# Performance work log

Hardware: AMD Instinct MI355X
Metric: run time of the kernel (lower is better)

## Reference

```python
import jax, jax.numpy as jnp
import numpy as np

NUM_CLASSES = 81
THRESH_HI = 0.5
THRESH_LO = 0.4
GAMMA = 2.0
ALPHA = 0.25
VARIANCE = (0.1, 0.2)  # cfg['variance'] in ssd.pytorch
B, P, T = 32, 24564, 20


def setup_inputs() -> dict:
    key = jax.random.key(0)
    k1, k2, k3, k4, k5, k6, k7 = jax.random.split(key, 7)
    loc_data = jax.random.normal(k1, (B, P, 4), jnp.float32)
    conf_data = jax.random.normal(k2, (B, P, NUM_CLASSES), jnp.float32)
    # priors in center form (cx, cy, w, h), all in [0,1]
    pcxy = jax.random.uniform(k3, (P, 2), minval=0.05, maxval=0.95)
    pwh = jax.random.uniform(k4, (P, 2), minval=0.04, maxval=0.5)
    priors = jnp.concatenate([pcxy, pwh], axis=-1).astype(jnp.float32)
    # ground-truth boxes in point form (xmin, ymin, xmax, ymax) + label
    tcxy = jax.random.uniform(k5, (B, T, 2), minval=0.1, maxval=0.9)
    twh = jax.random.uniform(k6, (B, T, 2), minval=0.05, maxval=0.4)
    boxes = jnp.clip(jnp.concatenate([tcxy - twh / 2, tcxy + twh / 2], -1), 0.0, 1.0)
    labels = jax.random.randint(k7, (B, T), 0, NUM_CLASSES - 1).astype(jnp.float32)
    targets = jnp.concatenate([boxes, labels[..., None]], axis=-1)  # [B,T,5]
    return {"loc_data": loc_data, "conf_data": conf_data, "priors": priors, "targets": targets}


def point_form(pr):
    # center form -> (xmin,ymin,xmax,ymax)
    return jnp.concatenate([pr[:, :2] - pr[:, 2:] / 2, pr[:, :2] + pr[:, 2:] / 2], -1)


def jaccard(box_a, box_b):
    # box_a [T,4], box_b [P,4], both point form -> IoU [T,P]
    lt = jnp.maximum(box_a[:, None, :2], box_b[None, :, :2])
    rb = jnp.minimum(box_a[:, None, 2:], box_b[None, :, 2:])
    wh = jnp.clip(rb - lt, 0.0)
    inter = wh[..., 0] * wh[..., 1]
    area_a = ((box_a[:, 2] - box_a[:, 0]) * (box_a[:, 3] - box_a[:, 1]))[:, None]
    area_b = ((box_b[:, 2] - box_b[:, 0]) * (box_b[:, 3] - box_b[:, 1]))[None, :]
    return inter / (area_a + area_b - inter)


def encode(matched, priors):
    # matched [P,4] point form, priors [P,4] center form
    g_cxcy = ((matched[:, :2] + matched[:, 2:]) / 2 - priors[:, :2]) / (VARIANCE[0] * priors[:, 2:])
    g_wh = jnp.log((matched[:, 2:] - matched[:, :2]) / priors[:, 2:]) / VARIANCE[1]
    return jnp.concatenate([g_cxcy, g_wh], -1)


def match_one(truths, labels, priors):
    # truths [T,4] point form, labels [T], priors [P,4] center form
    ov = jaccard(truths, point_form(priors))          # [T,P]
    best_prior_idx = jnp.argmax(ov, axis=1)           # [T] best prior per gt
    best_truth_overlap = jnp.max(ov, axis=0)          # [P]
    best_truth_idx = jnp.argmax(ov, axis=0)           # [P]
    # ensure every gt box keeps its best prior
    best_truth_overlap = best_truth_overlap.at[best_prior_idx].set(2.0)
    best_truth_idx = best_truth_idx.at[best_prior_idx].set(jnp.arange(truths.shape[0]))
    matched = truths[best_truth_idx]                  # [P,4]
    conf = labels[best_truth_idx].astype(jnp.int32) + 1
    conf = jnp.where(best_truth_overlap < THRESH_HI, -1, conf)  # ignore band
    conf = jnp.where(best_truth_overlap < THRESH_LO, 0, conf)   # background
    return encode(matched, priors), conf


def reference(loc_data, conf_data, priors, targets):
    truths = targets[..., :4]
    labels = targets[..., 4]
    loc_t, conf_t = jax.vmap(lambda t, l: match_one(t, l, priors))(truths, labels)
    pos = conf_t > 0                                  # [B,P]
    # smooth L1 over positive priors (sum reduction)
    diff = loc_data - loc_t
    ad = jnp.abs(diff)
    sl1 = jnp.where(ad < 1.0, 0.5 * diff * diff, ad - 0.5)
    loss_l = jnp.sum(sl1 * pos[..., None])
    # focal loss over ALL locations (ignore conf==-1)
    logits = conf_data.reshape(-1, NUM_CLASSES)
    tgt = conf_t.reshape(-1)
    valid = tgt >= 0
    tgt_safe = jnp.where(valid, tgt, 0)
    logpt = jnp.take_along_axis(jax.nn.log_softmax(logits, -1), tgt_safe[:, None], 1)[:, 0]
    pt = jnp.exp(logpt)
    alpha_t = jnp.where(tgt > 0, ALPHA, 1.0 - ALPHA)
    fl = -alpha_t * (1.0 - pt) ** GAMMA * logpt
    loss_c = jnp.sum(jnp.where(valid, fl, 0.0))
    n = jnp.sum(pos).astype(loc_data.dtype)
    return loss_l / n, loss_c / n
```

## Files before the change

kernel.cpp:

```cpp
#include <hip/hip_runtime.h>

#define NCLS 81
#define BB 32
#define PP 24564
#define TT 20
#define BP_SEGS 8
#define BP_SEG 3072
#define KL_BLOCKS 1792
#define KL_ROWS 32
#define KL_CHUNKS ((BB * PP) / KL_ROWS)
#define KL_F4 ((KL_ROWS * NCLS) / 4)

#define GLOAD_LDS16(g, l)                                                  \
    __builtin_amdgcn_global_load_lds(                                      \
        (const __attribute__((address_space(1))) void*)(g),                \
        (__attribute__((address_space(3))) void*)(l), 16, 0, 0)

__global__ __launch_bounds__(1024)
void k_bp(const float* __restrict__ priors,
          const float* __restrict__ targets,
          unsigned long long* __restrict__ bp_part,
          unsigned long long* __restrict__ bovbt)
{
    const int seg = blockIdx.x;
    const int b = blockIdx.y;

    __shared__ float trb[TT * 5];
    __shared__ unsigned long long wred[TT][16];
    if (threadIdx.x < TT * 5) trb[threadIdx.x] = targets[b * TT * 5 + threadIdx.x];
    __syncthreads();

    float X1[3], Y1[3], X2[3], Y2[3], pa[3];
    unsigned int pkey[3];
    bool ok[3];
    #pragma unroll
    for (int j = 0; j < 3; ++j) {
        int p = seg * BP_SEG + j * 1024 + threadIdx.x;
        ok[j] = p < PP;
        float4 pr = ok[j] ? ((const float4*)priors)[p] : make_float4(1.f, 1.f, 0.f, 0.f);
        float hw = __fmul_rn(pr.z, 0.5f), hh = __fmul_rn(pr.w, 0.5f);
        X1[j] = __fsub_rn(pr.x, hw); Y1[j] = __fsub_rn(pr.y, hh);
        X2[j] = __fadd_rn(pr.x, hw); Y2[j] = __fadd_rn(pr.y, hh);
        pa[j] = __fmul_rn(__fsub_rn(X2[j], X1[j]), __fsub_rn(Y2[j], Y1[j]));
        pkey[j] = 0xFFFFFFFFu - (unsigned)p;
    }

    const int wv = threadIdx.x >> 6;
    const int lane = threadIdx.x & 63;

    unsigned long long bkey[3] = {0ull, 0ull, 0ull};

    for (int t = 0; t < TT; ++t) {
        float tx1 = trb[t * 5 + 0], ty1 = trb[t * 5 + 1];
        float tx2 = trb[t * 5 + 2], ty2 = trb[t * 5 + 3];
        float ta = __fmul_rn(__fsub_rn(tx2, tx1), __fsub_rn(ty2, ty1));

        unsigned long long best = 0ull;
        #pragma unroll
        for (int j = 0; j < 3; ++j) {
            float lx = fmaxf(tx1, X1[j]), ly = fmaxf(ty1, Y1[j]);
            float rx = fminf(tx2, X2[j]), ry = fminf(ty2, Y2[j]);
            float w = fmaxf(__fsub_rn(rx, lx), 0.0f);
            float h = fmaxf(__fsub_rn(ry, ly), 0.0f);
            float inter = __fmul_rn(w, h);
            float denom = __fsub_rn(__fadd_rn(ta, pa[j]), inter);
            float ov = __fdiv_rn(inter, denom);
            unsigned long long ovhi = (unsigned long long)__float_as_uint(ov) << 32;
            unsigned long long key = ok[j] ? (ovhi | pkey[j]) : 0ull;
            if (key > best) best = key;
            unsigned long long rowk = ovhi | (unsigned long long)(31 - t);
            if (rowk > bkey[j]) bkey[j] = rowk;
        }
        #pragma unroll
        for (int s = 32; s; s >>= 1) {
            unsigned long long o = __shfl_xor(best, s, 64);
            if (o > best) best = o;
        }
        if (lane == 0) wred[t][wv] = best;
    }

    #pragma unroll
    for (int j = 0; j < 3; ++j) {
        int p = seg * BP_SEG + j * 1024 + threadIdx.x;
        if (p < PP) bovbt[b * PP + p] = bkey[j];
    }

    __syncthreads();
    if (threadIdx.x < TT) {
        unsigned long long m = wred[threadIdx.x][0];
        #pragma unroll
        for (int w = 1; w < 16; ++w) if (wred[threadIdx.x][w] > m) m = wred[threadIdx.x][w];
        bp_part[(b * TT + threadIdx.x) * BP_SEGS + seg] = m;
    }
}

__global__ __launch_bounds__(256, 4)
void k_stream(const float* __restrict__ conf,
              const float* __restrict__ loc,
              const float* __restrict__ priors,
              const float* __restrict__ targets,
              const unsigned long long* __restrict__ bp_part,
              const unsigned long long* __restrict__ bovbt,
              float* __restrict__ pl, float* __restrict__ pn, float* __restrict__ pc)
{
    __shared__ float buf[2][KL_ROWS * NCLS];
    __shared__ float trbS[2][2][TT * 5];
    __shared__ unsigned int bpbS[2][2][TT];

    const int tid = threadIdx.x;
    const int w = tid >> 6;
    const int lane = tid & 63;
    const int rl = tid >> 3;
    const int k = tid & 7;
    const float4* conf4 = (const float4*)conf;

    auto stage = [&](int c, int bi) {
        const float4* src = conf4 + (size_t)c * KL_F4;
        float4* dst = (float4*)buf[bi];
        #pragma unroll
        for (int j = 0; j < 2; ++j) {
            int idx = j * 256 + w * 64 + lane;
            GLOAD_LDS16(src + idx, dst + idx);
        }
        if (tid < KL_F4 - 512) {
            int idx = 512 + tid;
            GLOAD_LDS16(src + idx, dst + idx);
        }
    };

    auto load_meta = [&](int c, int bi) {
        int r0 = c * KL_ROWS;
        int b0 = r0 / PP;
        int b1 = (r0 + KL_ROWS - 1) / PP;
        if (tid < 200) {
            int which = tid / 100;
            int i = tid - which * 100;
            int bb = which ? b1 : b0;
            trbS[bi][which][i] = targets[bb * 100 + i];
        } else if (tid < 240) {
            int q2 = tid - 200;
            int which = q2 / 20;
            int t = q2 - which * 20;
            int bb = which ? b1 : b0;
            const unsigned long long* q = bp_part + (bb * TT + t) * BP_SEGS;
            unsigned long long m = q[0];
            #pragma unroll
            for (int s = 1; s < BP_SEGS; ++s) if (q[s] > m) m = q[s];
            bpbS[bi][which][t] = 0xFFFFFFFFu - (unsigned)(m & 0xFFFFFFFFull);
        }
    };

    const int c0 = blockIdx.x;
    stage(c0, 0);
    load_meta(c0, 0);
    __syncthreads();

    float accL = 0.0f, accN = 0.0f, accC = 0.0f;
    int cur = 0;

    for (int c = c0; c < KL_CHUNKS; c += KL_BLOCKS) {
        int cn = c + KL_BLOCKS;
        if (cn < KL_CHUNKS) {
            stage(cn, cur ^ 1);
            load_meta(cn, cur ^ 1);
        }

        int r = c * KL_ROWS + rl;
        unsigned long long rk = (k == 0) ? bovbt[r] : 0ull;

        const float* row = buf[cur] + rl * NCLS;
        float se = 0.0f;
        #pragma unroll
        for (int i = 0; i < 10; ++i) se += __expf(row[k * 10 + i]);
        if (k == 0) se += __expf(row[80]);
        se += __shfl_xor(se, 1, 8);
        se += __shfl_xor(se, 2, 8);
        se += __shfl_xor(se, 4, 8);

        int b0 = (c * KL_ROWS) / PP;
        int sel = (r >= (b0 + 1) * PP) ? 1 : 0;
        int p = r - (b0 + sel) * PP;
        const float* trb = &trbS[cur][sel][0];
        const unsigned int* bpb = &bpbS[cur][sel][0];

        int t0 = (k < 4) ? 3 * k : 12 + 2 * (k - 4);
        int nt = (k < 4) ? 3 : 2;
        int ft = -1;
        #pragma unroll
        for (int u = 0; u < 3; ++u) {
            if (u < nt) {
                int t = t0 + u;
                if (bpb[t] == (unsigned)p) ft = t;
            }
        }
        #pragma unroll
        for (int s = 4; s; s >>= 1) {
            int of = __shfl_xor(ft, s, 8);
            if (of > ft) ft = of;
        }

        if (k == 0) {
            int bt;
            float bov;
            if (ft >= 0) { bt = ft; bov = 2.0f; }
            else {
                bt = 31 - (int)(rk & 31ull);
                bov = __uint_as_float((unsigned)(rk >> 32));
            }
            int cc = (int)trb[bt * 5 + 4] + 1;
            if (bov < 0.5f) cc = -1;
            if (bov < 0.4f) cc = 0;

            if (cc > 0) {
                float4 pr = *(const float4*)(priors + p * 4);
                float mx1 = trb[bt * 5 + 0], my1 = trb[bt * 5 + 1];
                float mx2 = trb[bt * 5 + 2], my2 = trb[bt * 5 + 3];
                float cx = __fmul_rn(__fadd_rn(mx1, mx2), 0.5f);
                float cy = __fmul_rn(__fadd_rn(my1, my2), 0.5f);
                float gx = __fdiv_rn(__fsub_rn(cx, pr.x), __fmul_rn(0.1f, pr.z));
                float gy = __fdiv_rn(__fsub_rn(cy, pr.y), __fmul_rn(0.1f, pr.w));
                float gw = __fdiv_rn(logf(__fdiv_rn(__fsub_rn(mx2, mx1), pr.z)), 0.2f);
                float gh = __fdiv_rn(logf(__fdiv_rn(__fsub_rn(my2, my1), pr.w)), 0.2f);
                float4 ld = *(const float4*)(loc + (size_t)r * 4);
                float g0 = ld.x - gx, g1 = ld.y - gy, g2 = ld.z - gw, g3 = ld.w - gh;
                float a0 = fabsf(g0), a1 = fabsf(g1), a2 = fabsf(g2), a3 = fabsf(g3);
                accL += (a0 < 1.0f) ? 0.5f * g0 * g0 : (a0 - 0.5f);
                accL += (a1 < 1.0f) ? 0.5f * g1 * g1 : (a1 - 0.5f);
                accL += (a2 < 1.0f) ? 0.5f * g2 * g2 : (a2 - 0.5f);
                accL += (a3 < 1.0f) ? 0.5f * g3 * g3 : (a3 - 0.5f);
                accN += 1.0f;
            }
            if (cc >= 0) {
                float xt = row[cc];
                float logpt = xt - __logf(se);
                float pt = __expf(logpt);
                float at = (cc > 0) ? 0.25f : 0.75f;
                float om = 1.0f - pt;
                accC -= at * om * om * logpt;
            }
        }
        __syncthreads();
        cur ^= 1;
    }

    float* red = &trbS[0][0][0];
    red[tid] = accL;
    __syncthreads();
    for (int s = 128; s; s >>= 1) {
        if (tid < s) red[tid] += red[tid + s];
        __syncthreads();
    }
    if (tid == 0) pl[blockIdx.x] = red[0];
    __syncthreads();

    red[tid] = accN;
    __syncthreads();
    for (int s = 128; s; s >>= 1) {
        if (tid < s) red[tid] += red[tid + s];
        __syncthreads();
    }
    if (tid == 0) pn[blockIdx.x] = red[0];
    __syncthreads();

    red[tid] = accC;
    __syncthreads();
    for (int s = 128; s; s >>= 1) {
        if (tid < s) red[tid] += red[tid + s];
        __syncthreads();
    }
    if (tid == 0) pc[blockIdx.x] = red[0];
}

__global__ __launch_bounds__(256)
void k_final(const float* __restrict__ pl, const float* __restrict__ pn,
             const float* __restrict__ pc, float* __restrict__ out)
{
    __shared__ float sl[256], sc[256], sn[256];
    float L = 0.0f, C = 0.0f, N = 0.0f;
    for (int i = threadIdx.x; i < KL_BLOCKS; i += 256) {
        L += pl[i]; N += pn[i]; C += pc[i];
    }
    sl[threadIdx.x] = L; sc[threadIdx.x] = C; sn[threadIdx.x] = N;
    __syncthreads();
    for (int s = 128; s; s >>= 1) {
        if (threadIdx.x < s) {
            sl[threadIdx.x] += sl[threadIdx.x + s];
            sc[threadIdx.x] += sc[threadIdx.x + s];
            sn[threadIdx.x] += sn[threadIdx.x + s];
        }
        __syncthreads();
    }
    if (threadIdx.x == 0) {
        out[0] = sl[0] / sn[0];
        out[1] = sc[0] / sn[0];
    }
}

extern "C" void kernel_launch(void* const* d_in, const int* in_sizes, int n_in,
                              void* d_out, int out_size, void* d_ws, size_t ws_size,
                              hipStream_t stream)
{
    const float* loc     = (const float*)d_in[0];
    const float* conf    = (const float*)d_in[1];
    const float* priors  = (const float*)d_in[2];
    const float* targets = (const float*)d_in[3];
    float* out = (float*)d_out;

    char* ws = (char*)d_ws;
    unsigned long long* bp_part = (unsigned long long*)ws;
    unsigned long long* bovbt   = (unsigned long long*)(ws + 65536);
    float* pl = (float*)(ws + 65536 + 6291456);
    float* pn = pl + KL_BLOCKS;
    float* pc = pn + KL_BLOCKS;

    k_bp<<<dim3(BP_SEGS, BB), 1024, 0, stream>>>(priors, targets, bp_part, bovbt);
    k_stream<<<KL_BLOCKS, 256, 0, stream>>>(conf, loc, priors, targets, bp_part,
                                            bovbt, pl, pn, pc);
    k_final<<<1, 256, 0, stream>>>(pl, pn, pc, out);
}
```

Baseline: 82.96 us.

## Make streaming kernel wave-independent with per-wave double buffering and prefetched metadata

Restructures the streaming kernel so that each wave owns an 8-row chunk and its own double-buffered LDS slice, with explicit vmcnt waits in place of block-wide __syncthreads per iteration. The per-row bovbt, prior and loc values are prefetched one iteration ahead, and all targets and best-prior indices are loaded into LDS once per block. The per-segment best-prior reduction moves into k_bp via 64-bit atomicMax after a memset, and the grid drops to 1024 blocks. This aims to remove barrier stalls and metadata reloads, but it relies on hand-counted vmcnt values that must match the number of outstanding loads, and it adds a memset launch.

```diff
diff --git a/kernel.cpp b/kernel.cpp
--- a/kernel.cpp
+++ b/kernel.cpp
@@ -6,10 +6,9 @@
 #define TT 20
 #define BP_SEGS 8
 #define BP_SEG 3072
-#define KL_BLOCKS 1792
-#define KL_ROWS 32
-#define KL_CHUNKS ((BB * PP) / KL_ROWS)
-#define KL_F4 ((KL_ROWS * NCLS) / 4)
+#define NBLK 1024
+#define NWAVES (NBLK * 4)
+#define WC_TOTAL ((BB * PP) / 8)
 
 #define GLOAD_LDS16(g, l)                                                  \
     __builtin_amdgcn_global_load_lds(                                      \
@@ -19,7 +18,7 @@
 __global__ __launch_bounds__(1024)
 void k_bp(const float* __restrict__ priors,
           const float* __restrict__ targets,
-          unsigned long long* __restrict__ bp_part,
+          unsigned long long* __restrict__ bp_final,
           unsigned long long* __restrict__ bovbt)
 {
     const int seg = blockIdx.x;
@@ -90,7 +89,7 @@
         unsigned long long m = wred[threadIdx.x][0];
         #pragma unroll
         for (int w = 1; w < 16; ++w) if (wred[threadIdx.x][w] > m) m = wred[threadIdx.x][w];
-        bp_part[(b * TT + threadIdx.x) * BP_SEGS + seg] = m;
+        atomicMax(&bp_final[b * TT + threadIdx.x], m);
     }
 }
 
@@ -99,76 +98,77 @@
               const float* __restrict__ loc,
               const float* __restrict__ priors,
               const float* __restrict__ targets,
-              const unsigned long long* __restrict__ bp_part,
+              const unsigned long long* __restrict__ bp_final,
               const unsigned long long* __restrict__ bovbt,
               float* __restrict__ pl, float* __restrict__ pn, float* __restrict__ pc)
 {
-    __shared__ float buf[2][KL_ROWS * NCLS];
-    __shared__ float trbS[2][2][TT * 5];
-    __shared__ unsigned int bpbS[2][2][TT];
+    __shared__ float buf[4][2][8 * NCLS];
+    __shared__ float trbAll[BB * TT * 5];
+    __shared__ unsigned int bpAll[BB * TT];
+    __shared__ float red[256];
 
     const int tid = threadIdx.x;
-    const int w = tid >> 6;
+    const int wv = tid >> 6;
     const int lane = tid & 63;
-    const int rl = tid >> 3;
-    const int k = tid & 7;
+    const int rloc = lane >> 3;
+    const int k = lane & 7;
     const float4* conf4 = (const float4*)conf;
 
-    auto stage = [&](int c, int bi) {
-        const float4* src = conf4 + (size_t)c * KL_F4;
-        float4* dst = (float4*)buf[bi];
-        #pragma unroll
-        for (int j = 0; j < 2; ++j) {
-            int idx = j * 256 + w * 64 + lane;
-            GLOAD_LDS16(src + idx, dst + idx);
-        }
-        if (tid < KL_F4 - 512) {
-            int idx = 512 + tid;
-            GLOAD_LDS16(src + idx, dst + idx);
-        }
+    for (int i = tid; i < BB * TT * 5; i += 256) trbAll[i] = targets[i];
+    for (int i = tid; i < BB * TT; i += 256)
+        bpAll[i] = 0xFFFFFFFFu - (unsigned)(bp_final[i] & 0xFFFFFFFFull);
+    __syncthreads();
+
+    auto stage = [&](int wc, int bi) {
+        const float4* src = conf4 + (size_t)wc * 162;
+        float4* dst = (float4*)(&buf[wv][bi][0]);
+        GLOAD_LDS16(src + lane, dst + lane);
+        GLOAD_LDS16(src + 64 + lane, dst + 64 + lane);
+        if (lane < 34) GLOAD_LDS16(src + 128 + lane, dst + 128 + lane);
     };
 
-    auto load_meta = [&](int c, int bi) {
-        int r0 = c * KL_ROWS;
+    const int gw = blockIdx.x * 4 + wv;
+    float accL = 0.0f, accN = 0.0f, accC = 0.0f;
+
+    int wc = gw;
+    int cur = 0;
+    unsigned long long rk = 0ull;
+    float4 pr4 = make_float4(0.f, 0.f, 1.f, 1.f);
+    float4 ld4 = make_float4(0.f, 0.f, 0.f, 0.f);
+    {
+        stage(wc, 0);
+        int r0 = wc * 8 + rloc;
         int b0 = r0 / PP;
-        int b1 = (r0 + KL_ROWS - 1) / PP;
-        if (tid < 200) {
-            int which = tid / 100;
-            int i = tid - which * 100;
-            int bb = which ? b1 : b0;
-            trbS[bi][which][i] = targets[bb * 100 + i];
-        } else if (tid < 240) {
-            int q2 = tid - 200;
-            int which = q2 / 20;
-            int t = q2 - which * 20;
-            int bb = which ? b1 : b0;
-            const unsigned long long* q = bp_part + (bb * TT + t) * BP_SEGS;
-            unsigned long long m = q[0];
-            #pragma unroll
-            for (int s = 1; s < BP_SEGS; ++s) if (q[s] > m) m = q[s];
-            bpbS[bi][which][t] = 0xFFFFFFFFu - (unsigned)(m & 0xFFFFFFFFull);
-        }
-    };
-
-    const int c0 = blockIdx.x;
-    stage(c0, 0);
-    load_meta(c0, 0);
-    __syncthreads();
-
-    float accL = 0.0f, accN = 0.0f, accC = 0.0f;
-    int cur = 0;
-
-    for (int c = c0; c < KL_CHUNKS; c += KL_BLOCKS) {
-        int cn = c + KL_BLOCKS;
-        if (cn < KL_CHUNKS) {
-            stage(cn, cur ^ 1);
-            load_meta(cn, cur ^ 1);
-        }
-
-        int r = c * KL_ROWS + rl;
-        unsigned long long rk = (k == 0) ? bovbt[r] : 0ull;
-
-        const float* row = buf[cur] + rl * NCLS;
+        int p0 = r0 - b0 * PP;
+        if (k == 0) {
+            rk = bovbt[r0];
+            pr4 = *(const float4*)(priors + p0 * 4);
+            ld4 = *(const float4*)(loc + (size_t)r0 * 4);
+        }
+    }
+
+    for (; wc < WC_TOTAL; wc += NWAVES) {
+        const int wn = wc + NWAVES;
+        const bool hasnext = wn < WC_TOTAL;
+        unsigned long long rkn = 0ull;
+        float4 pr4n = pr4, ld4n = ld4;
+        if (hasnext) {
+            stage(wn, cur ^ 1);
+            int rn = wn * 8 + rloc;
+            int bn = rn / PP;
+            int pn_ = rn - bn * PP;
+            if (k == 0) {
+                rkn = bovbt[rn];
+                pr4n = *(const float4*)(priors + pn_ * 4);
+                ld4n = *(const float4*)(loc + (size_t)rn * 4);
+            }
+        }
+        __builtin_amdgcn_sched_barrier(0);
+        if (hasnext) asm volatile("s_waitcnt vmcnt(6)" ::: "memory");
+        else         asm volatile("s_waitcnt vmcnt(0)" ::: "memory");
+        __builtin_amdgcn_sched_barrier(0);
+
+        const float* row = &buf[wv][cur][0] + rloc * NCLS;
         float se = 0.0f;
         #pragma unroll
         for (int i = 0; i < 10; ++i) se += __expf(row[k * 10 + i]);
@@ -177,11 +177,11 @@
         se += __shfl_xor(se, 2, 8);
         se += __shfl_xor(se, 4, 8);
 
-        int b0 = (c * KL_ROWS) / PP;
-        int sel = (r >= (b0 + 1) * PP) ? 1 : 0;
-        int p = r - (b0 + sel) * PP;
-        const float* trb = &trbS[cur][sel][0];
-        const unsigned int* bpb = &bpbS[cur][sel][0];
+        const int r = wc * 8 + rloc;
+        const int b = r / PP;
+        const int p = r - b * PP;
+        const unsigned int* bpb = &bpAll[b * TT];
+        const float* trb = &trbAll[b * TT * 5];
 
         int t0 = (k < 4) ? 3 * k : 12 + 2 * (k - 4);
         int nt = (k < 4) ? 3 : 2;
@@ -212,17 +212,15 @@
             if (bov < 0.4f) cc = 0;
 
             if (cc > 0) {
-                float4 pr = *(const float4*)(priors + p * 4);
                 float mx1 = trb[bt * 5 + 0], my1 = trb[bt * 5 + 1];
                 float mx2 = trb[bt * 5 + 2], my2 = trb[bt * 5 + 3];
                 float cx = __fmul_rn(__fadd_rn(mx1, mx2), 0.5f);
                 float cy = __fmul_rn(__fadd_rn(my1, my2), 0.5f);
-                float gx = __fdiv_rn(__fsub_rn(cx, pr.x), __fmul_rn(0.1f, pr.z));
-                float gy = __fdiv_rn(__fsub_rn(cy, pr.y), __fmul_rn(0.1f, pr.w));
-                float gw = __fdiv_rn(logf(__fdiv_rn(__fsub_rn(mx2, mx1), pr.z)), 0.2f);
-                float gh = __fdiv_rn(logf(__fdiv_rn(__fsub_rn(my2, my1), pr.w)), 0.2f);
-                float4 ld = *(const float4*)(loc + (size_t)r * 4);
-                float g0 = ld.x - gx, g1 = ld.y - gy, g2 = ld.z - gw, g3 = ld.w - gh;
+                float gx = __fdiv_rn(__fsub_rn(cx, pr4.x), __fmul_rn(0.1f, pr4.z));
+                float gy = __fdiv_rn(__fsub_rn(cy, pr4.y), __fmul_rn(0.1f, pr4.w));
+                float gw_ = __fdiv_rn(logf(__fdiv_rn(__fsub_rn(mx2, mx1), pr4.z)), 0.2f);
+                float gh_ = __fdiv_rn(logf(__fdiv_rn(__fsub_rn(my2, my1), pr4.w)), 0.2f);
+                float g0 = ld4.x - gx, g1 = ld4.y - gy, g2 = ld4.z - gw_, g3 = ld4.w - gh_;
                 float a0 = fabsf(g0), a1 = fabsf(g1), a2 = fabsf(g2), a3 = fabsf(g3);
                 accL += (a0 < 1.0f) ? 0.5f * g0 * g0 : (a0 - 0.5f);
                 accL += (a1 < 1.0f) ? 0.5f * g1 * g1 : (a1 - 0.5f);
@@ -239,11 +237,11 @@
                 accC -= at * om * om * logpt;
             }
         }
-        __syncthreads();
+        rk = rkn; pr4 = pr4n; ld4 = ld4n;
         cur ^= 1;
     }
 
-    float* red = &trbS[0][0][0];
+    __syncthreads();
     red[tid] = accL;
     __syncthreads();
     for (int s = 128; s; s >>= 1) {
@@ -277,7 +275,7 @@
 {
     __shared__ float sl[256], sc[256], sn[256];
     float L = 0.0f, C = 0.0f, N = 0.0f;
-    for (int i = threadIdx.x; i < KL_BLOCKS; i += 256) {
+    for (int i = threadIdx.x; i < NBLK; i += 256) {
         L += pl[i]; N += pn[i]; C += pc[i];
     }
     sl[threadIdx.x] = L; sc[threadIdx.x] = C; sn[threadIdx.x] = N;
@@ -307,14 +305,15 @@
     float* out = (float*)d_out;
 
     char* ws = (char*)d_ws;
-    unsigned long long* bp_part = (unsigned long long*)ws;
-    unsigned long long* bovbt   = (unsigned long long*)(ws + 65536);
+    unsigned long long* bp_final = (unsigned long long*)ws;
+    unsigned long long* bovbt    = (unsigned long long*)(ws + 65536);
     float* pl = (float*)(ws + 65536 + 6291456);
-    float* pn = pl + KL_BLOCKS;
-    float* pc = pn + KL_BLOCKS;
-
-    k_bp<<<dim3(BP_SEGS, BB), 1024, 0, stream>>>(priors, targets, bp_part, bovbt);
-    k_stream<<<KL_BLOCKS, 256, 0, stream>>>(conf, loc, priors, targets, bp_part,
-                                            bovbt, pl, pn, pc);
+    float* pn = pl + NBLK;
+    float* pc = pn + NBLK;
+
+    hipMemsetAsync(bp_final, 0, BB * TT * sizeof(unsigned long long), stream);
+    k_bp<<<dim3(BP_SEGS, BB), 1024, 0, stream>>>(priors, targets, bp_final, bovbt);
+    k_stream<<<NBLK, 256, 0, stream>>>(conf, loc, priors, targets, bp_final,
+                                       bovbt, pl, pn, pc);
     k_final<<<1, 256, 0, stream>>>(pl, pn, pc, out);
 }
```

Measured after the change: 89.25 us. 1.08x slower.

## Fold forced matches into bovbt and batch per-row loss work across chunks

Applied to the files above, without the earlier changes.

A tiny new kernel writes each truth's best prior directly into bovbt as a forced match, so the streaming kernel no longer compares every row against per-truth best priors. The streaming kernel now keeps all targets in LDS, stores per-row sum-exp and target logit in shared memory, and runs the match/encode/loss work in bursts of 8 chunks using all 256 threads instead of one thread in eight. The grid shrinks from 1792 to 1024 blocks. The cost is an extra serial launch, more LDS use, and a forced-match write order that may differ from the reference when two truths share the same best prior.

```diff
diff --git a/kernel.cpp b/kernel.cpp
--- a/kernel.cpp
+++ b/kernel.cpp
@@ -6,7 +6,7 @@
 #define TT 20
 #define BP_SEGS 8
 #define BP_SEG 3072
-#define KL_BLOCKS 1792
+#define KL_BLOCKS 1024
 #define KL_ROWS 32
 #define KL_CHUNKS ((BB * PP) / KL_ROWS)
 #define KL_F4 ((KL_ROWS * NCLS) / 4)
@@ -94,18 +94,37 @@
     }
 }
 
+__global__ __launch_bounds__(64)
+void k_fold(const unsigned long long* __restrict__ bp_part,
+            unsigned long long* __restrict__ bovbt)
+{
+    int b = threadIdx.x;
+    if (b < BB) {
+        for (int t = 0; t < TT; ++t) {
+            const unsigned long long* q = bp_part + (b * TT + t) * BP_SEGS;
+            unsigned long long m = q[0];
+            #pragma unroll
+            for (int s = 1; s < BP_SEGS; ++s) if (q[s] > m) m = q[s];
+            unsigned p = 0xFFFFFFFFu - (unsigned)(m & 0xFFFFFFFFull);
+            bovbt[(size_t)b * PP + p] =
+                (0x40000000ull << 32) | (unsigned long long)(31 - t);
+        }
+    }
+}
+
 __global__ __launch_bounds__(256, 4)
 void k_stream(const float* __restrict__ conf,
               const float* __restrict__ loc,
               const float* __restrict__ priors,
               const float* __restrict__ targets,
-              const unsigned long long* __restrict__ bp_part,
               const unsigned long long* __restrict__ bovbt,
               float* __restrict__ pl, float* __restrict__ pn, float* __restrict__ pc)
 {
     __shared__ float buf[2][KL_ROWS * NCLS];
-    __shared__ float trbS[2][2][TT * 5];
-    __shared__ unsigned int bpbS[2][2][TT];
+    __shared__ float trbAll[BB * TT * 5];
+    __shared__ float seb[256], xtb[256];
+    __shared__ int sidx[8];
+    __shared__ float red[256];
 
     const int tid = threadIdx.x;
     const int w = tid >> 6;
@@ -128,89 +147,29 @@
         }
     };
 
-    auto load_meta = [&](int c, int bi) {
-        int r0 = c * KL_ROWS;
-        int b0 = r0 / PP;
-        int b1 = (r0 + KL_ROWS - 1) / PP;
-        if (tid < 200) {
-            int which = tid / 100;
-            int i = tid - which * 100;
-            int bb = which ? b1 : b0;
-            trbS[bi][which][i] = targets[bb * 100 + i];
-        } else if (tid < 240) {
-            int q2 = tid - 200;
-            int which = q2 / 20;
-            int t = q2 - which * 20;
-            int bb = which ? b1 : b0;
-            const unsigned long long* q = bp_part + (bb * TT + t) * BP_SEGS;
-            unsigned long long m = q[0];
-            #pragma unroll
-            for (int s = 1; s < BP_SEGS; ++s) if (q[s] > m) m = q[s];
-            bpbS[bi][which][t] = 0xFFFFFFFFu - (unsigned)(m & 0xFFFFFFFFull);
-        }
-    };
+    for (int i = tid; i < BB * TT * 5; i += 256) trbAll[i] = targets[i];
 
     const int c0 = blockIdx.x;
     stage(c0, 0);
-    load_meta(c0, 0);
     __syncthreads();
 
     float accL = 0.0f, accN = 0.0f, accC = 0.0f;
-    int cur = 0;
-
-    for (int c = c0; c < KL_CHUNKS; c += KL_BLOCKS) {
-        int cn = c + KL_BLOCKS;
-        if (cn < KL_CHUNKS) {
-            stage(cn, cur ^ 1);
-            load_meta(cn, cur ^ 1);
-        }
-
-        int r = c * KL_ROWS + rl;
-        unsigned long long rk = (k == 0) ? bovbt[r] : 0ull;
-
-        const float* row = buf[cur] + rl * NCLS;
-        float se = 0.0f;
-        #pragma unroll
-        for (int i = 0; i < 10; ++i) se += __expf(row[k * 10 + i]);
-        if (k == 0) se += __expf(row[80]);
-        se += __shfl_xor(se, 1, 8);
-        se += __shfl_xor(se, 2, 8);
-        se += __shfl_xor(se, 4, 8);
-
-        int b0 = (c * KL_ROWS) / PP;
-        int sel = (r >= (b0 + 1) * PP) ? 1 : 0;
-        int p = r - (b0 + sel) * PP;
-        const float* trb = &trbS[cur][sel][0];
-        const unsigned int* bpb = &bpbS[cur][sel][0];
-
-        int t0 = (k < 4) ? 3 * k : 12 + 2 * (k - 4);
-        int nt = (k < 4) ? 3 : 2;
-        int ft = -1;
-        #pragma unroll
-        for (int u = 0; u < 3; ++u) {
-            if (u < nt) {
-                int t = t0 + u;
-                if (bpb[t] == (unsigned)p) ft = t;
-            }
-        }
-        #pragma unroll
-        for (int s = 4; s; s >>= 1) {
-            int of = __shfl_xor(ft, s, 8);
-            if (of > ft) ft = of;
-        }
-
-        if (k == 0) {
-            int bt;
-            float bov;
-            if (ft >= 0) { bt = ft; bov = 2.0f; }
-            else {
-                bt = 31 - (int)(rk & 31ull);
-                bov = __uint_as_float((unsigned)(rk >> 32));
-            }
+    int cur = 0, na = 0;
+
+    auto burst = [&](int n) {
+        int span = tid >> 5;
+        if (span < n) {
+            int r = sidx[span] * KL_ROWS + (tid & 31);
+            int b = r / PP;
+            int p = r - b * PP;
+            const float* trb = &trbAll[b * TT * 5];
+            unsigned long long rk = bovbt[r];
+            int bt = 31 - (int)(rk & 31ull);
+            float bov = __uint_as_float((unsigned)(rk >> 32));
             int cc = (int)trb[bt * 5 + 4] + 1;
             if (bov < 0.5f) cc = -1;
             if (bov < 0.4f) cc = 0;
-
+            int si = span * 32 + (tid & 31);
             if (cc > 0) {
                 float4 pr = *(const float4*)(priors + p * 4);
                 float mx1 = trb[bt * 5 + 0], my1 = trb[bt * 5 + 1];
@@ -231,8 +190,7 @@
                 accN += 1.0f;
             }
             if (cc >= 0) {
-                float xt = row[cc];
-                float logpt = xt - __logf(se);
+                float logpt = xtb[si] - __logf(seb[si]);
                 float pt = __expf(logpt);
                 float at = (cc > 0) ? 0.25f : 0.75f;
                 float om = 1.0f - pt;
@@ -240,10 +198,42 @@
             }
         }
         __syncthreads();
+    };
+
+    for (int c = c0; c < KL_CHUNKS; c += KL_BLOCKS) {
+        int cn = c + KL_BLOCKS;
+        if (cn < KL_CHUNKS) stage(cn, cur ^ 1);
+
+        int r = c * KL_ROWS + rl;
+        unsigned long long rk = (k == 0) ? bovbt[r] : 0ull;
+
+        const float* row = buf[cur] + rl * NCLS;
+        float se = 0.0f;
+        #pragma unroll
+        for (int i = 0; i < 10; ++i) se += __expf(row[k * 10 + i]);
+        if (k == 0) se += __expf(row[80]);
+        se += __shfl_xor(se, 1, 8);
+        se += __shfl_xor(se, 2, 8);
+        se += __shfl_xor(se, 4, 8);
+
+        if (k == 0) {
+            int b = r / PP;
+            int bt = 31 - (int)(rk & 31ull);
+            float bov = __uint_as_float((unsigned)(rk >> 32));
+            int cc = (int)trbAll[b * TT * 5 + bt * 5 + 4] + 1;
+            if (bov < 0.5f) cc = -1;
+            if (bov < 0.4f) cc = 0;
+            seb[na * 32 + rl] = se;
+            xtb[na * 32 + rl] = row[cc < 0 ? 0 : cc];
+        }
+        if (tid == 0) sidx[na] = c;
+        __syncthreads();
+        ++na;
+        if (na == 8) { burst(8); na = 0; }
         cur ^= 1;
     }
-
-    float* red = &trbS[0][0][0];
+    if (na > 0) burst(na);
+
     red[tid] = accL;
     __syncthreads();
     for (int s = 128; s; s >>= 1) {
@@ -314,7 +304,8 @@
     float* pc = pn + KL_BLOCKS;
 
     k_bp<<<dim3(BP_SEGS, BB), 1024, 0, stream>>>(priors, targets, bp_part, bovbt);
-    k_stream<<<KL_BLOCKS, 256, 0, stream>>>(conf, loc, priors, targets, bp_part,
-                                            bovbt, pl, pn, pc);
+    k_fold<<<1, 64, 0, stream>>>(bp_part, bovbt);
+    k_stream<<<KL_BLOCKS, 256, 0, stream>>>(conf, loc, priors, targets, bovbt,
+                                            pl, pn, pc);
     k_final<<<1, 256, 0, stream>>>(pl, pn, pc, out);
 }
```

New measurement: 81.26 us (median of 4 runs). -2.1%, faster.
